# Kernel tuning notes

Measured on AMD Instinct MI355X. Metric: run time of the kernel, lower is better.

Reference implementation:

```python
import jax, jax.numpy as jnp
import numpy as np

N_EMBD = 1024
HEAD_SIZE = 128
B, T = 8, 2048


def apply_rope(x):
    # x: (B, T, D); rotate interleaved pairs, matching torch view(B,T,D//2,2)
    b, t, d = x.shape
    freqs = 1.0 / (10000.0 ** (jnp.arange(0, d, 2, dtype=jnp.float32) / d))  # (D//2,)
    angles = jnp.arange(t, dtype=jnp.float32)[:, None] * freqs[None, :]      # (T, D//2)
    cos_a = jnp.cos(angles).astype(x.dtype)
    sin_a = jnp.sin(angles).astype(x.dtype)
    xr = x.reshape(b, t, d // 2, 2)
    x0, x1 = xr[..., 0], xr[..., 1]
    rot = jnp.stack([x0 * cos_a - x1 * sin_a, x0 * sin_a + x1 * cos_a], axis=-1)
    return rot.reshape(b, t, d)


def setup_inputs() -> dict:
    key = jax.random.key(0)
    kx, kq, kk, kv = jax.random.split(key, 4)
    x = jax.random.normal(kx, (B, T, N_EMBD), dtype=jnp.float32)
    scale = 0.02
    Wq = jax.random.normal(kq, (N_EMBD, HEAD_SIZE), dtype=jnp.float32) * scale
    Wk = jax.random.normal(kk, (N_EMBD, HEAD_SIZE), dtype=jnp.float32) * scale
    Wv = jax.random.normal(kv, (N_EMBD, HEAD_SIZE), dtype=jnp.float32) * scale
    return {"x": x, "Wq": Wq, "Wk": Wk, "Wv": Wv}


def reference(x, Wq, Wk, Wv):
    # QKV projections (bias=False)
    q = x @ Wq  # (B, T, H)
    k = x @ Wk
    v = x @ Wv
    q = apply_rope(q)
    k = apply_rope(k)
    d = k.shape[-1]
    wei = jnp.einsum('bqd,bkd->bqk', q, k) * (d ** -0.5)  # (B, T, T)
    causal = jnp.tril(jnp.ones((q.shape[1], q.shape[1]), dtype=bool))
    wei = jnp.where(causal, wei, jnp.finfo(wei.dtype).min)
    wei = jax.nn.softmax(wei, axis=-1)
    out = jnp.einsum('bqk,bkd->bqd', wei, v)  # (B, T, H)
    return out
```

## Files before the change

kernel.cpp:

```cpp
#include <hip/hip_runtime.h>
#include <math.h>

#define BB 8
#define TT 2048
#define EE 1024
#define DD 128

typedef _Float16 f16x8 __attribute__((ext_vector_type(8)));
typedef _Float16 f16x4 __attribute__((ext_vector_type(4)));
typedef float    f32x4 __attribute__((ext_vector_type(4)));
typedef float    f32x16 __attribute__((ext_vector_type(16)));

#define QSCALE 0.12752406f


__global__ __launch_bounds__(256)
void wt_prep_kernel(const float* __restrict__ Wq,
                    const float* __restrict__ Wk,
                    const float* __restrict__ Wv,
                    _Float16* __restrict__ Wb)
{
    int gid = blockIdx.x * 256 + threadIdx.x;
    int kc  = gid / 768;
    int rem = gid - kc * 768;
    int ns  = rem >> 6;
    int ln  = rem & 63;
    int n   = ns * 32 + (ln & 31);
    int k0  = kc * 16 + (ln >> 5) * 8;
    const float* __restrict__ W = (n < 128) ? Wq : (n < 256) ? Wk : Wv;
    int nl = n & 127;
    f16x8 w;
#pragma unroll
    for (int j = 0; j < 8; j++)
        w[j] = (_Float16)W[(size_t)(k0 + j) * DD + nl];
    *(f16x8*)&Wb[(size_t)gid * 8] = w;
}

__global__ __launch_bounds__(512)
void proj_rope_kernel(const float* __restrict__ x,
                      const _Float16* __restrict__ Wb,
                      _Float16* __restrict__ Qb,
                      _Float16* __restrict__ Ka,
                      _Float16* __restrict__ Va)
{
    const int r0   = blockIdx.x * 64;
    const int tid  = threadIdx.x;
    const int wave = tid >> 6;
    const int lane = tid & 63;
    const int half = lane >> 5;
    const int col  = lane & 31;
    const int wave_m = wave & 1;
    const int wave_n = wave >> 1;

    __shared__ _Float16 Xb[2][4096];
    __shared__ _Float16 Out[64][136];

    f32x16 acc[3];
#pragma unroll
    for (int s = 0; s < 3; s++) acc[s] = (f32x16)0.f;

    const int sr = tid >> 3;
    const int sc = (tid & 7) * 4;
    const float* __restrict__ xp = &x[(size_t)(r0 + sr) * EE + sc];
    const int sm = sr >> 5, rr = sr & 31;
    const int w0 = (((sc      >> 4) * 2 + sm) << 9) + ((rr + 32 * ((sc       >> 3) & 1)) << 3) + (sc & 7);
    const int w1 = ((((sc+32) >> 4) * 2 + sm) << 9) + ((rr + 32 * (((sc+32)  >> 3) & 1)) << 3) + (sc & 7);

    float4 pa0 = *(const float4*)(xp);
    float4 pa1 = *(const float4*)(xp + 32);
    {
        f16x4 h0 = { (_Float16)pa0.x, (_Float16)pa0.y, (_Float16)pa0.z, (_Float16)pa0.w };
        f16x4 h1 = { (_Float16)pa1.x, (_Float16)pa1.y, (_Float16)pa1.z, (_Float16)pa1.w };
        *(f16x4*)&Xb[0][w0] = h0;
        *(f16x4*)&Xb[0][w1] = h1;
    }
    float4 na0 = *(const float4*)(xp + 64);
    float4 na1 = *(const float4*)(xp + 96);

    for (int it = 0; it < 16; it++) {
        const int buf = it & 1;
        __syncthreads();
#pragma unroll
        for (int kc = 0; kc < 4; kc++) {
            f16x8 a = *(f16x8*)&Xb[buf][((kc * 2 + wave_m) << 9) + lane * 8];
#pragma unroll
            for (int s = 0; s < 3; s++) {
                f16x8 b = *(const f16x8*)&Wb[((size_t)(it * 4 + kc) * 12 + wave_n * 3 + s) * 512 + lane * 8];
                acc[s] = __builtin_amdgcn_mfma_f32_32x32x16_f16(a, b, acc[s], 0, 0, 0);
            }
        }
        if (it + 1 < 16) {
            f16x4 h0 = { (_Float16)na0.x, (_Float16)na0.y, (_Float16)na0.z, (_Float16)na0.w };
            f16x4 h1 = { (_Float16)na1.x, (_Float16)na1.y, (_Float16)na1.z, (_Float16)na1.w };
            *(f16x4*)&Xb[buf ^ 1][w0] = h0;
            *(f16x4*)&Xb[buf ^ 1][w1] = h1;
        }
        if (it + 2 < 16) {
            na0 = *(const float4*)(xp + (it + 2) * 64);
            na1 = *(const float4*)(xp + (it + 2) * 64 + 32);
        }
    }

    const int bidx = r0 >> 11;
    const int t0   = r0 & (TT - 1);

    for (int p = 0; p < 3; p++) {
        __syncthreads();
#pragma unroll
        for (int s = 0; s < 3; s++) {
            int gs = wave_n * 3 + s;
            if ((gs >> 2) != p) continue;
            int dcol = (gs & 3) * 32 + col;
            float f = 0.f;
            if (p < 2)
                f = __powf(10000.0f, -(float)(dcol & ~1) * (1.0f / 128.0f));
#pragma unroll
            for (int rg = 0; rg < 16; rg++) {
                int mrow = wave_m * 32 + (rg & 3) + 8 * (rg >> 2) + 4 * half;
                float av = acc[s][rg];
                float res;
                if (p < 2) {
                    float ap = __shfl_xor(av, 1);
                    float sa, ca;
                    __sincosf((float)(t0 + mrow) * f, &sa, &ca);
                    res = av * ca + ap * ((dcol & 1) ? sa : -sa);
                    if (p == 0) res *= QSCALE;
                } else {
                    res = av;
                }
                Out[mrow][dcol] = (_Float16)res;
            }
        }
        __syncthreads();
        if (p < 2) {
            _Float16* __restrict__ dst = (p == 0) ? Qb : Ka;
#pragma unroll
            for (int jj = 0; jj < 2; jj++) {
                int cid = tid + 512 * jj;
                int sl = cid >> 9, kc = (cid >> 6) & 7, ln = cid & 63;
                f16x8 v8 = *(f16x8*)&Out[sl * 32 + (ln & 31)][kc * 16 + (ln >> 5) * 8];
                size_t ga = ((((size_t)bidx * 64 + (t0 >> 5) + sl) * 8 + kc) * 64 + ln) * 8;
                *(f16x8*)&dst[ga] = v8;
            }
        } else {
#pragma unroll
            for (int jj = 0; jj < 2; jj++) {
                int cid = tid + 512 * jj;
                int kcl = cid >> 8, ds = (cid >> 6) & 3, ln = cid & 63;
                f16x8 vv;
#pragma unroll
                for (int e = 0; e < 8; e++)
                    vv[e] = Out[kcl * 16 + (ln >> 5) * 8 + e][ds * 32 + (ln & 31)];
                size_t ga = ((((size_t)bidx * 128 + (t0 >> 4) + kcl) * 4 + ds) * 64 + ln) * 8;
                *(f16x8*)&Va[ga] = vv;
            }
        }
    }
}

__global__ __launch_bounds__(256)
void attn_kernel(const _Float16* __restrict__ Qb,
                 const _Float16* __restrict__ Ka,
                 const _Float16* __restrict__ Va,
                 _Float16* __restrict__ opart,
                 float* __restrict__ mpart,
                 float* __restrict__ lpart)
{
    const int b  = blockIdx.y;
    const int v_ = 39 - blockIdx.x;
    int xt, c;
    if (v_ < 4)       { xt = v_;                  c = 0; }
    else if (v_ < 12) { xt = 4 + ((v_ - 4) >> 1); c = (v_ - 4) & 1; }
    else if (v_ < 24) { xt = 8 + (v_ - 12) / 3;   c = (v_ - 12) % 3; }
    else              { xt = 12 + ((v_ - 24) >> 2); c = (v_ - 24) & 3; }
    const int q0 = xt * 128;
    const int nt = 2 * xt + 2;
    const int kt_begin = c * 8;
    const int kt_end   = (kt_begin + 8 < nt) ? (kt_begin + 8) : nt;

    const int tid  = threadIdx.x;
    const int wave = tid >> 6;
    const int lane = tid & 63;
    const int half = lane >> 5;
    const int col  = lane & 31;

    __shared__ _Float16 Kb[8192];
    __shared__ _Float16 Vb[8192];
    __shared__ _Float16 Ps[4][32][72];

    const _Float16* __restrict__ kst = Ka + (size_t)b * 64 * 4096;
    const _Float16* __restrict__ vst = Va + (size_t)b * 128 * 2048;

    const int qg = q0 + wave * 32 + col;
    f16x8 qb[8];
#pragma unroll
    for (int kc = 0; kc < 8; kc++)
        qb[kc] = *(const f16x8*)&Qb[((((size_t)b * 64 + xt * 4 + wave) * 8 + kc) * 64 + lane) * 8];

    f32x16 Of[4];
#pragma unroll
    for (int t = 0; t < 4; t++) Of[t] = (f32x16)0.f;
    float m_ = -1e30f, l_ = 0.f;

    f16x8 kr[4], vr[4];
    {
        const _Float16* kp = kst + (size_t)kt_begin * 8192;
        const _Float16* vp = vst + (size_t)kt_begin * 8192;
#pragma unroll
        for (int i = 0; i < 4; i++) kr[i] = *(const f16x8*)&kp[(tid + 256 * i) * 8];
#pragma unroll
        for (int i = 0; i < 4; i++) vr[i] = *(const f16x8*)&vp[(tid + 256 * i) * 8];
    }

    for (int kt = kt_begin; kt < kt_end; kt++) {
        const int kb0 = kt * 64;
        __syncthreads();
#pragma unroll
        for (int i = 0; i < 4; i++) *(f16x8*)&Kb[(tid + 256 * i) * 8] = kr[i];
#pragma unroll
        for (int i = 0; i < 4; i++) *(f16x8*)&Vb[(tid + 256 * i) * 8] = vr[i];
        __syncthreads();
        if (kt + 1 < kt_end) {
            const _Float16* kp = kst + (size_t)(kt + 1) * 8192;
            const _Float16* vp = vst + (size_t)(kt + 1) * 8192;
#pragma unroll
            for (int i = 0; i < 4; i++) kr[i] = *(const f16x8*)&kp[(tid + 256 * i) * 8];
#pragma unroll
            for (int i = 0; i < 4; i++) vr[i] = *(const f16x8*)&vp[(tid + 256 * i) * 8];
        }

        f32x16 sf[2];
#pragma unroll
        for (int g = 0; g < 2; g++) {
            sf[g] = (f32x16)0.f;
#pragma unroll
            for (int kc = 0; kc < 8; kc++) {
                f16x8 kf = *(f16x8*)&Kb[((g * 8 + kc) * 64 + lane) * 8];
                sf[g] = __builtin_amdgcn_mfma_f32_32x32x16_f16(kf, qb[kc], sf[g], 0, 0, 0);
            }
        }

        const bool diag = (kt >= 2 * xt);
        float mloc = -1e30f;
#pragma unroll
        for (int g = 0; g < 2; g++)
#pragma unroll
            for (int rg = 0; rg < 16; rg++) {
                int key = kb0 + g * 32 + (rg & 3) + 8 * (rg >> 2) + 4 * half;
                float val = sf[g][rg];
                val = (!diag || key <= qg) ? val : -1e30f;
                sf[g][rg] = val;
                mloc = fmaxf(mloc, val);
            }
        mloc = fmaxf(mloc, __shfl_xor(mloc, 32));
        float mnew  = fmaxf(m_, mloc);
        float alpha = __builtin_amdgcn_exp2f(m_ - mnew);
        float ps = 0.f;
#pragma unroll
        for (int g = 0; g < 2; g++) {
#pragma unroll
            for (int rc = 0; rc < 4; rc++) {
                f16x4 p4;
#pragma unroll
                for (int rr = 0; rr < 4; rr++) {
                    float p = __builtin_amdgcn_exp2f(sf[g][4 * rc + rr] - mnew);
                    ps += p;
                    p4[rr] = (_Float16)p;
                }
                *(f16x4*)&Ps[wave][col][g * 32 + 8 * rc + 4 * half] = p4;
            }
        }
        ps += __shfl_xor(ps, 32);
        l_ = l_ * alpha + ps;
        m_ = mnew;
#pragma unroll
        for (int t = 0; t < 4; t++) Of[t] *= alpha;

        f16x8 pb[4];
#pragma unroll
        for (int kc = 0; kc < 4; kc++)
            pb[kc] = *(f16x8*)&Ps[wave][col][kc * 16 + half * 8];
#pragma unroll
        for (int t = 0; t < 4; t++) {
#pragma unroll
            for (int kcl = 0; kcl < 4; kcl++) {
                f16x8 vf = *(f16x8*)&Vb[((kcl * 4 + t) * 64 + lane) * 8];
                Of[t] = __builtin_amdgcn_mfma_f32_32x32x16_f16(vf, pb[kcl], Of[t], 0, 0, 0);
            }
        }
    }

    const int slot = (b * 16 + xt) * 4 + c;
    _Float16* op = opart + ((size_t)slot * 128 + wave * 32 + col) * DD;
#pragma unroll
    for (int t = 0; t < 4; t++) {
#pragma unroll
        for (int rc = 0; rc < 4; rc++) {
            f16x4 o4 = { (_Float16)Of[t][4 * rc + 0], (_Float16)Of[t][4 * rc + 1],
                         (_Float16)Of[t][4 * rc + 2], (_Float16)Of[t][4 * rc + 3] };
            *(f16x4*)&op[t * 32 + 8 * rc + 4 * half] = o4;
        }
    }
    if (half == 0) {
        mpart[slot * 128 + wave * 32 + col] = m_;
        lpart[slot * 128 + wave * 32 + col] = l_;
    }
}

__global__ __launch_bounds__(256)
void combine_kernel(const _Float16* __restrict__ opart,
                    const float* __restrict__ mpart,
                    const float* __restrict__ lpart,
                    float* __restrict__ out)
{
    int gid = blockIdx.x * 256 + threadIdx.x;
    int d   = gid & 127;
    int t   = gid >> 7;
    int b   = t >> 11;
    int tl  = t & (TT - 1);
    int xt  = tl >> 7;
    int rl  = tl & 127;
    int np  = (2 * xt + 2 + 7) >> 3;
    int sb  = (b * 16 + xt) * 4;

    float mm = -1e30f;
    for (int j = 0; j < np; j++)
        mm = fmaxf(mm, mpart[(sb + j) * 128 + rl]);
    float acc = 0.f, den = 0.f;
    for (int j = 0; j < np; j++) {
        float w = __builtin_amdgcn_exp2f(mpart[(sb + j) * 128 + rl] - mm);
        den += w * lpart[(sb + j) * 128 + rl];
        acc += w * (float)opart[((size_t)(sb + j) * 128 + rl) * DD + d];
    }
    out[gid] = acc / den;
}

extern "C" void kernel_launch(void* const* d_in, const int* in_sizes, int n_in,
                              void* d_out, int out_size, void* d_ws, size_t ws_size,
                              hipStream_t stream)
{
    const float* x  = (const float*)d_in[0];
    const float* Wq = (const float*)d_in[1];
    const float* Wk = (const float*)d_in[2];
    const float* Wv = (const float*)d_in[3];
    float* out = (float*)d_out;

    const size_t NTOK = (size_t)BB * TT;
    _Float16* Qb = (_Float16*)d_ws;
    _Float16* Ka = Qb + NTOK * DD;
    _Float16* Va = Ka + NTOK * DD;
    _Float16* Wb = Va + NTOK * DD;
    _Float16* opart = Wb + (size_t)384 * EE;
    float* mp = (float*)(opart + (size_t)512 * 128 * DD);
    float* lp = mp + 512 * 128;

    wt_prep_kernel<<<dim3(192), dim3(256), 0, stream>>>(Wq, Wk, Wv, Wb);
    proj_rope_kernel<<<dim3(256), dim3(512), 0, stream>>>(x, Wb, Qb, Ka, Va);
    attn_kernel<<<dim3(40, BB), dim3(256), 0, stream>>>(Qb, Ka, Va, opart, mp, lp);
    combine_kernel<<<dim3((int)(NTOK * DD / 256)), dim3(256), 0, stream>>>(opart, mp, lp, out);
}
```

Baseline: 164.8 us.

## Split attention KV range into 4-tile chunks and register-prefetch projection weights

The attention split-K chunk size drops from 8 to 4 KV tiles, so the grid grows from 40 to 72 blocks per batch. This raises parallelism and evens out load across the causal triangle, at the cost of more partial outputs for the combine kernel to merge. The projection kernel now double-buffers its weight fragments in registers, prefetching the next iteration's weights before the MFMAs instead of loading them inline, with the loop fully unrolled. Barriers are replaced by a custom inline-asm barrier that waits only on LDS counters, which may let pending global loads stay in flight across the barrier.

```diff
diff --git a/kernel.cpp b/kernel.cpp
--- a/kernel.cpp
+++ b/kernel.cpp
@@ -12,6 +12,8 @@
 typedef float    f32x16 __attribute__((ext_vector_type(16)));
 
 #define QSCALE 0.12752406f
+
+#define BAR() asm volatile("s_waitcnt lgkmcnt(0)\n\ts_barrier" ::: "memory")
 
 
 __global__ __launch_bounds__(256)
@@ -66,38 +68,51 @@
     const int w0 = (((sc      >> 4) * 2 + sm) << 9) + ((rr + 32 * ((sc       >> 3) & 1)) << 3) + (sc & 7);
     const int w1 = ((((sc+32) >> 4) * 2 + sm) << 9) + ((rr + 32 * (((sc+32)  >> 3) & 1)) << 3) + (sc & 7);
 
-    float4 pa0 = *(const float4*)(xp);
-    float4 pa1 = *(const float4*)(xp + 32);
     {
-        f16x4 h0 = { (_Float16)pa0.x, (_Float16)pa0.y, (_Float16)pa0.z, (_Float16)pa0.w };
-        f16x4 h1 = { (_Float16)pa1.x, (_Float16)pa1.y, (_Float16)pa1.z, (_Float16)pa1.w };
+        float4 c0 = *(const float4*)(xp);
+        float4 c1 = *(const float4*)(xp + 32);
+        f16x4 h0 = { (_Float16)c0.x, (_Float16)c0.y, (_Float16)c0.z, (_Float16)c0.w };
+        f16x4 h1 = { (_Float16)c1.x, (_Float16)c1.y, (_Float16)c1.z, (_Float16)c1.w };
         *(f16x4*)&Xb[0][w0] = h0;
         *(f16x4*)&Xb[0][w1] = h1;
     }
-    float4 na0 = *(const float4*)(xp + 64);
-    float4 na1 = *(const float4*)(xp + 96);
-
+    float4 n0 = *(const float4*)(xp + 64);
+    float4 n1 = *(const float4*)(xp + 96);
+
+    f16x8 Wr[2][12];
+#pragma unroll
+    for (int kc = 0; kc < 4; kc++)
+#pragma unroll
+        for (int s = 0; s < 3; s++)
+            Wr[0][kc * 3 + s] = *(const f16x8*)&Wb[((size_t)kc * 12 + wave_n * 3 + s) * 512 + lane * 8];
+
+#pragma unroll
     for (int it = 0; it < 16; it++) {
-        const int buf = it & 1;
-        __syncthreads();
+        BAR();
+        if (it + 1 < 16) {
+#pragma unroll
+            for (int kc = 0; kc < 4; kc++)
+#pragma unroll
+                for (int s = 0; s < 3; s++)
+                    Wr[(it + 1) & 1][kc * 3 + s] = *(const f16x8*)&Wb[
+                        ((size_t)((it + 1) * 4 + kc) * 12 + wave_n * 3 + s) * 512 + lane * 8];
+        }
 #pragma unroll
         for (int kc = 0; kc < 4; kc++) {
-            f16x8 a = *(f16x8*)&Xb[buf][((kc * 2 + wave_m) << 9) + lane * 8];
-#pragma unroll
-            for (int s = 0; s < 3; s++) {
-                f16x8 b = *(const f16x8*)&Wb[((size_t)(it * 4 + kc) * 12 + wave_n * 3 + s) * 512 + lane * 8];
-                acc[s] = __builtin_amdgcn_mfma_f32_32x32x16_f16(a, b, acc[s], 0, 0, 0);
-            }
+            f16x8 a = *(f16x8*)&Xb[it & 1][((kc * 2 + wave_m) << 9) + lane * 8];
+#pragma unroll
+            for (int s = 0; s < 3; s++)
+                acc[s] = __builtin_amdgcn_mfma_f32_32x32x16_f16(a, Wr[it & 1][kc * 3 + s], acc[s], 0, 0, 0);
         }
         if (it + 1 < 16) {
-            f16x4 h0 = { (_Float16)na0.x, (_Float16)na0.y, (_Float16)na0.z, (_Float16)na0.w };
-            f16x4 h1 = { (_Float16)na1.x, (_Float16)na1.y, (_Float16)na1.z, (_Float16)na1.w };
-            *(f16x4*)&Xb[buf ^ 1][w0] = h0;
-            *(f16x4*)&Xb[buf ^ 1][w1] = h1;
+            f16x4 h0 = { (_Float16)n0.x, (_Float16)n0.y, (_Float16)n0.z, (_Float16)n0.w };
+            f16x4 h1 = { (_Float16)n1.x, (_Float16)n1.y, (_Float16)n1.z, (_Float16)n1.w };
+            *(f16x4*)&Xb[(it + 1) & 1][w0] = h0;
+            *(f16x4*)&Xb[(it + 1) & 1][w1] = h1;
         }
         if (it + 2 < 16) {
-            na0 = *(const float4*)(xp + (it + 2) * 64);
-            na1 = *(const float4*)(xp + (it + 2) * 64 + 32);
+            n0 = *(const float4*)(xp + (it + 2) * 64);
+            n1 = *(const float4*)(xp + (it + 2) * 64 + 32);
         }
     }
 
@@ -166,17 +181,18 @@
                  float* __restrict__ mpart,
                  float* __restrict__ lpart)
 {
-    const int b  = blockIdx.y;
-    const int v_ = 39 - blockIdx.x;
-    int xt, c;
-    if (v_ < 4)       { xt = v_;                  c = 0; }
-    else if (v_ < 12) { xt = 4 + ((v_ - 4) >> 1); c = (v_ - 4) & 1; }
-    else if (v_ < 24) { xt = 8 + (v_ - 12) / 3;   c = (v_ - 12) % 3; }
-    else              { xt = 12 + ((v_ - 24) >> 2); c = (v_ - 24) & 3; }
+    const int b = blockIdx.y;
+    int rem = blockIdx.x, xt = 15;
+    while (true) {
+        int nc = (xt + 2) >> 1;
+        if (rem < nc) break;
+        rem -= nc; xt--;
+    }
+    const int c = rem;
     const int q0 = xt * 128;
     const int nt = 2 * xt + 2;
-    const int kt_begin = c * 8;
-    const int kt_end   = (kt_begin + 8 < nt) ? (kt_begin + 8) : nt;
+    const int kt_begin = c * 4;
+    const int kt_end   = (kt_begin + 4 < nt) ? (kt_begin + 4) : nt;
 
     const int tid  = threadIdx.x;
     const int wave = tid >> 6;
@@ -214,12 +230,12 @@
 
     for (int kt = kt_begin; kt < kt_end; kt++) {
         const int kb0 = kt * 64;
-        __syncthreads();
+        BAR();
 #pragma unroll
         for (int i = 0; i < 4; i++) *(f16x8*)&Kb[(tid + 256 * i) * 8] = kr[i];
 #pragma unroll
         for (int i = 0; i < 4; i++) *(f16x8*)&Vb[(tid + 256 * i) * 8] = vr[i];
-        __syncthreads();
+        BAR();
         if (kt + 1 < kt_end) {
             const _Float16* kp = kst + (size_t)(kt + 1) * 8192;
             const _Float16* vp = vst + (size_t)(kt + 1) * 8192;
@@ -290,7 +306,7 @@
         }
     }
 
-    const int slot = (b * 16 + xt) * 4 + c;
+    const int slot = b * 72 + (((xt + 1) * (xt + 1)) >> 2) + c;
     _Float16* op = opart + ((size_t)slot * 128 + wave * 32 + col) * DD;
 #pragma unroll
     for (int t = 0; t < 4; t++) {
@@ -320,8 +336,8 @@
     int tl  = t & (TT - 1);
     int xt  = tl >> 7;
     int rl  = tl & 127;
-    int np  = (2 * xt + 2 + 7) >> 3;
-    int sb  = (b * 16 + xt) * 4;
+    int np  = (xt + 2) >> 1;
+    int sb  = b * 72 + (((xt + 1) * (xt + 1)) >> 2);
 
     float mm = -1e30f;
     for (int j = 0; j < np; j++)
@@ -351,11 +367,11 @@
     _Float16* Va = Ka + NTOK * DD;
     _Float16* Wb = Va + NTOK * DD;
     _Float16* opart = Wb + (size_t)384 * EE;
-    float* mp = (float*)(opart + (size_t)512 * 128 * DD);
-    float* lp = mp + 512 * 128;
+    float* mp = (float*)(opart + (size_t)576 * 128 * DD);
+    float* lp = mp + 576 * 128;
 
     wt_prep_kernel<<<dim3(192), dim3(256), 0, stream>>>(Wq, Wk, Wv, Wb);
     proj_rope_kernel<<<dim3(256), dim3(512), 0, stream>>>(x, Wb, Qb, Ka, Va);
-    attn_kernel<<<dim3(40, BB), dim3(256), 0, stream>>>(Qb, Ka, Va, opart, mp, lp);
+    attn_kernel<<<dim3(72, BB), dim3(256), 0, stream>>>(Qb, Ka, Va, opart, mp, lp);
     combine_kernel<<<dim3((int)(NTOK * DD / 256)), dim3(256), 0, stream>>>(opart, mp, lp, out);
 }
```

Measured after the change: 173.7 us. 1.05x slower.
